# Kernel optimization log

Measured on AMD Instinct MI355X. Metric: run time of the kernel, lower is better.

The kernel has to match this reference:

```python
import jax, jax.numpy as jnp
import numpy as np

B, V, W, H = 512, 256, 64, 64  # batch, num_variables, window, hidden_size


def setup_inputs() -> dict:
    key = jax.random.key(0)
    ks = jax.random.split(key, 10)
    s = 0.05
    return {
        "x": jax.random.normal(ks[0], (B, V, W), dtype=jnp.float32),
        # nn.LSTM(input=V, hidden=H): gate order i, f, g, o
        "w_ih": jax.random.normal(ks[1], (4 * H, V), dtype=jnp.float32) * s,
        "w_hh": jax.random.normal(ks[2], (4 * H, H), dtype=jnp.float32) * s,
        "b_ih": jax.random.normal(ks[3], (4 * H,), dtype=jnp.float32) * s,
        "b_hh": jax.random.normal(ks[4], (4 * H,), dtype=jnp.float32) * s,
        # linear_v: Linear(window, 1, bias=False)
        "w_v": jax.random.normal(ks[5], (1, W), dtype=jnp.float32) * s,
        # linear_w: Linear(2H, window)
        "w_w": jax.random.normal(ks[6], (W, 2 * H), dtype=jnp.float32) * s,
        "b_w": jax.random.normal(ks[7], (W,), dtype=jnp.float32) * s,
        # linear_u: Linear(window, window)
        "w_u": jax.random.normal(ks[8], (W, W), dtype=jnp.float32) * s,
        "b_u": jax.random.normal(ks[9], (W,), dtype=jnp.float32) * s,
    }


def reference(x, w_ih, w_hh, b_ih, b_hh, w_v, w_w, b_w, w_u, b_u):
    batch, n_var, window = x.shape
    hidden = w_hh.shape[1]
    # linear_u over the window (last) dim: (B, V, W)
    u_out = jnp.einsum("bvw,uw->bvu", x, w_u) + b_u
    x_steps = jnp.transpose(x, (2, 0, 1))  # (W, B, V)

    def step(carry, x_t):
        h, c = carry  # each (B, H)
        # input attention
        wout = jnp.concatenate([h, c], axis=1) @ w_w.T + b_w          # (B, W)
        score = jnp.einsum("bvw,w->bv", jnp.tanh(wout[:, None, :] + u_out), w_v[0])
        alpha = jax.nn.softmax(score, axis=1)                          # (B, V)
        x_tilde = alpha * x_t                                          # (B, V)
        # LSTM cell (torch gate order i, f, g, o)
        gates = x_tilde @ w_ih.T + b_ih + h @ w_hh.T + b_hh            # (B, 4H)
        i_g, f_g, g_g, o_g = jnp.split(gates, 4, axis=1)
        i_g = jax.nn.sigmoid(i_g)
        f_g = jax.nn.sigmoid(f_g)
        g_g = jnp.tanh(g_g)
        o_g = jax.nn.sigmoid(o_g)
        c_new = f_g * c + i_g * g_g
        h_new = o_g * jnp.tanh(c_new)
        return (h_new, c_new), (x_tilde, h_new)

    init = (jnp.zeros((batch, hidden), x.dtype), jnp.zeros((batch, hidden), x.dtype))
    _, (x_tilde_seq, h_seq) = jax.lax.scan(step, init, x_steps)
    # matches torch.stack(x_tilde_list) (W,B,V) and torch.stack(h_list) (W,B,H)
    return x_tilde_seq, h_seq
```

## Files before the change

### kernel.cpp

```cpp
#include <hip/hip_runtime.h>


#define KLOG2E  1.4426950408889634f
#define K2LOG2E 2.8853900817779268f

typedef _Float16 h2 __attribute__((ext_vector_type(2)));
union H2U { h2 h; unsigned u; };

__device__ __forceinline__ float frcp(float x)  { return __builtin_amdgcn_rcpf(x); }
__device__ __forceinline__ float fexp2(float x) { return __builtin_amdgcn_exp2f(x); }
__device__ __forceinline__ float fsigmoid(float x) { return frcp(1.f + fexp2(-KLOG2E * x)); }
__device__ __forceinline__ float ftanh(float x) { return 1.f - 2.f * frcp(fexp2(K2LOG2E * x) + 1.f); }

#if __has_builtin(__builtin_amdgcn_fdot2)
__device__ __forceinline__ float fdot2(h2 a, h2 b, float c) { return __builtin_amdgcn_fdot2(a, b, c, false); }
#else
__device__ __forceinline__ float fdot2(h2 a, h2 b, float c) { return c + (float)a.x*(float)b.x + (float)a.y*(float)b.y; }
#endif

__device__ __forceinline__ h2 pkrtz(float a, float b) {
#if __has_builtin(__builtin_amdgcn_cvt_pkrtz)
    return __builtin_bit_cast(h2, __builtin_amdgcn_cvt_pkrtz(a, b));
#else
    h2 r; r.x = (_Float16)a; r.y = (_Float16)b; return r;
#endif
}

#define L_EA   0
#define L_EB   17408
#define L_PSA  34816
#define L_PSB  36864
#define L_XTA  38912
#define L_XTB  39168
#define L_XHA  39424
#define L_XHB  39552
#define L_EWA  39680
#define L_EWB  39744
#define L_HCA  39808
#define L_HCB  39936
#define L_BI   40064
#define L_WV   40320
#define L_TOT  40384

__global__ __launch_bounds__(512, 2) void enc_kernel(
    const float* __restrict__ x,
    const float* __restrict__ w_ih,
    const float* __restrict__ w_hh,
    const float* __restrict__ b_ih,
    const float* __restrict__ b_hh,
    const float* __restrict__ w_v,
    const float* __restrict__ w_w,
    const float* __restrict__ b_w,
    const float* __restrict__ w_u,
    const float* __restrict__ b_u,
    float* __restrict__ out_xt,
    float* __restrict__ out_h)
{
    extern __shared__ float lds[];
    float* EA  = lds + L_EA;   float* EB  = lds + L_EB;
    float* psA = lds + L_PSA;  float* psB = lds + L_PSB;
    float* xtA = lds + L_XTA;  float* xtB = lds + L_XTB;
    float* xhA = lds + L_XHA;  float* xhB = lds + L_XHB;
    float* ewA = lds + L_EWA;  float* ewB = lds + L_EWB;
    float* hcA = lds + L_HCA;  float* hcB = lds + L_HCB;
    float* biasL = lds + L_BI;
    float* wv2L  = lds + L_WV;

    const int tid  = threadIdx.x;
    const int lane = tid & 63;
    const int wvi  = tid >> 6;
    const int bA   = blockIdx.x;
    const int bB   = blockIdx.x + 256;

    h2    wihr2[64];
    float whhr[32];
    {
        const int jg = lane, sg = wvi;
#pragma unroll
        for (int jj = 0; jj < 4; ++jj) {
            const float4* g4 = (const float4*)(w_ih + (jg + 64*jj)*256 + sg*32);
#pragma unroll
            for (int i = 0; i < 8; ++i) {
                float4 v4 = g4[i];
                wihr2[jj*16 + 2*i + 0] = pkrtz(v4.x, v4.y);
                wihr2[jj*16 + 2*i + 1] = pkrtz(v4.z, v4.w);
            }
            const float4* h4 = (const float4*)(w_hh + (jg + 64*jj)*64 + sg*8);
            float4 u0 = h4[0], u1 = h4[1];
            whhr[jj*8 + 0] = u0.x; whhr[jj*8 + 1] = u0.y;
            whhr[jj*8 + 2] = u0.z; whhr[jj*8 + 3] = u0.w;
            whhr[jj*8 + 4] = u1.x; whhr[jj*8 + 5] = u1.y;
            whhr[jj*8 + 6] = u1.z; whhr[jj*8 + 7] = u1.w;
        }
    }
    const int w8 = wvi*8 + (lane & 7);
    const int kg = lane >> 3;
    float4 www4[4];
#pragma unroll
    for (int m = 0; m < 4; ++m)
        www4[m] = *(const float4*)&w_w[w8*128 + kg*4 + 32*m];
    const float bwr = b_w[w8];
    float Sv = 0.f;
#pragma unroll
    for (int wi = 0; wi < 64; ++wi) Sv += w_v[wi];
    const float bu_lane = b_u[lane];

    if (tid < 256) biasL[tid] = b_ih[tid] + b_hh[tid];
    if (tid < 64) wv2L[tid] = -2.f * w_v[tid];
    if (tid < 128) hcA[tid] = 0.f;
    else if (tid < 256) hcB[tid - 128] = 0.f;

#pragma unroll 1
    for (int bb = 0; bb < 2; ++bb) {
        float* E = bb ? EB : EA;
        const int b = bb ? bB : bA;
#pragma unroll 1
        for (int half = 0; half < 2; ++half) {
            float4 wu_r[8];
#pragma unroll
            for (int i = 0; i < 8; ++i)
                wu_r[i] = *(const float4*)&w_u[lane*64 + half*32 + 4*i];
            const float* xb = x + b*16384 + half*32;
#pragma unroll 2
            for (int vi = 0; vi < 32; ++vi) {
                int v = __builtin_amdgcn_readfirstlane(wvi*32 + vi);
                const float4* xr = (const float4*)(xb + v*64);
                float acc = 0.f;
#pragma unroll
                for (int i = 0; i < 8; ++i) {
                    float4 xx = xr[i]; float4 wu = wu_r[i];
                    acc += xx.x*wu.x + xx.y*wu.y + xx.z*wu.z + xx.w*wu.w;
                }
                if (half == 0) E[v*68 + lane] = acc + bu_lane;
                else           E[v*68 + lane] = fexp2(K2LOG2E * (E[v*68 + lane] + acc));
            }
        }
    }
    __syncthreads();

    const int  xj   = tid & 255;
    const int  bsel = tid >> 8;
    const float* xrow = x + (bsel ? bB : bA)*16384 + xj*64;
    float*       psX  = bsel ? psB : psA;
    const float* Erow = (bsel ? EB : EA) + xj*68;
    const float* ewX  = bsel ? ewB : ewA;
    float xcur = xrow[0];

    for (int t = 0; t < 64; ++t) {
        {
            float accA = 0.f, accB = 0.f;
#pragma unroll
            for (int m = 0; m < 4; ++m) {
                float4 w4 = www4[m];
                float4 hA = *(const float4*)&hcA[kg*4 + 32*m];
                float4 hB = *(const float4*)&hcB[kg*4 + 32*m];
                accA += hA.x*w4.x + hA.y*w4.y + hA.z*w4.z + hA.w*w4.w;
                accB += hB.x*w4.x + hB.y*w4.y + hB.z*w4.z + hB.w*w4.w;
            }
#pragma unroll
            for (int off = 8; off <= 32; off <<= 1) {
                accA += __shfl_xor(accA, off, 64);
                accB += __shfl_xor(accB, off, 64);
            }
            if (kg == 0)      ewA[w8] = fexp2(K2LOG2E * (accA + bwr));
            else if (kg == 1) ewB[w8] = fexp2(K2LOG2E * (accB + bwr));
        }
        float xnxt = (t < 63) ? xrow[t + 1] : 0.f;
        __syncthreads();

        {
            float acc = Sv;
#pragma unroll
            for (int q = 0; q < 16; ++q) {
                float4 e4 = *(const float4*)&Erow[4*q];
                float4 c4 = *(const float4*)&ewX[4*q];
                float4 v4 = *(const float4*)&wv2L[4*q];
                acc += v4.x * frcp(e4.x*c4.x + 1.f);
                acc += v4.y * frcp(e4.y*c4.y + 1.f);
                acc += v4.z * frcp(e4.z*c4.z + 1.f);
                acc += v4.w * frcp(e4.w*c4.w + 1.f);
            }
            float e = fexp2(KLOG2E * acc);
            psX[xj]       = e;
            psX[256 + xj] = e * xcur;
        }
        xcur = xnxt;
        __syncthreads();

        if (wvi < 2) {
            float* ps = wvi ? psB : psA;
            float* xt = wvi ? xtB : xtA;
            unsigned* xh = (unsigned*)(wvi ? xhB : xhA);
            float4 ev = *(const float4*)&ps[4*lane];
            float4 ex = *(const float4*)&ps[256 + 4*lane];
            float sum = (ev.x + ev.y) + (ev.z + ev.w);
#pragma unroll
            for (int off = 1; off <= 32; off <<= 1) sum += __shfl_xor(sum, off, 64);
            float r = frcp(sum);
            float4 xo;
            xo.x = ex.x*r; xo.y = ex.y*r; xo.z = ex.z*r; xo.w = ex.w*r;
            *(float4*)&xt[4*lane] = xo;
            H2U p0, p1;
            p0.h = pkrtz(xo.x, xo.y);
            p1.h = pkrtz(xo.z, xo.w);
            xh[2*lane]     = p0.u;
            xh[2*lane + 1] = p1.u;
        }
        __syncthreads();

        {
            float xtv = bsel ? xtB[xj] : xtA[xj];
            out_xt[t*131072 + (bsel ? bB : bA)*256 + xj] = xtv;

            const int sg = wvi, jg = lane;
            float aA[4] = {0.f, 0.f, 0.f, 0.f};
            float aB[4] = {0.f, 0.f, 0.f, 0.f};
            const uint4* xA = (const uint4*)xhA + sg*4;
            const uint4* xB = (const uint4*)xhB + sg*4;
#pragma unroll
            for (int i = 0; i < 4; ++i) {
                uint4 ua = xA[i], ub = xB[i];
                H2U u0, u1, u2, u3, v0, v1, v2, v3;
                u0.u = ua.x; u1.u = ua.y; u2.u = ua.z; u3.u = ua.w;
                v0.u = ub.x; v1.u = ub.y; v2.u = ub.z; v3.u = ub.w;
#pragma unroll
                for (int jj = 0; jj < 4; ++jj) {
                    aA[jj] = fdot2(u0.h, wihr2[jj*16 + 4*i + 0], aA[jj]);
                    aA[jj] = fdot2(u1.h, wihr2[jj*16 + 4*i + 1], aA[jj]);
                    aA[jj] = fdot2(u2.h, wihr2[jj*16 + 4*i + 2], aA[jj]);
                    aA[jj] = fdot2(u3.h, wihr2[jj*16 + 4*i + 3], aA[jj]);
                    aB[jj] = fdot2(v0.h, wihr2[jj*16 + 4*i + 0], aB[jj]);
                    aB[jj] = fdot2(v1.h, wihr2[jj*16 + 4*i + 1], aB[jj]);
                    aB[jj] = fdot2(v2.h, wihr2[jj*16 + 4*i + 2], aB[jj]);
                    aB[jj] = fdot2(v3.h, wihr2[jj*16 + 4*i + 3], aB[jj]);
                }
            }
            float4 hA0 = *(const float4*)&hcA[sg*8];
            float4 hA1 = *(const float4*)&hcA[sg*8 + 4];
            float4 hB0 = *(const float4*)&hcB[sg*8];
            float4 hB1 = *(const float4*)&hcB[sg*8 + 4];
#pragma unroll
            for (int jj = 0; jj < 4; ++jj) {
                aA[jj] += hA0.x*whhr[jj*8+0] + hA0.y*whhr[jj*8+1] + hA0.z*whhr[jj*8+2] + hA0.w*whhr[jj*8+3]
                        + hA1.x*whhr[jj*8+4] + hA1.y*whhr[jj*8+5] + hA1.z*whhr[jj*8+6] + hA1.w*whhr[jj*8+7];
                aB[jj] += hB0.x*whhr[jj*8+0] + hB0.y*whhr[jj*8+1] + hB0.z*whhr[jj*8+2] + hB0.w*whhr[jj*8+3]
                        + hB1.x*whhr[jj*8+4] + hB1.y*whhr[jj*8+5] + hB1.z*whhr[jj*8+6] + hB1.w*whhr[jj*8+7];
            }
            psA[sg*256 + jg      ] = aA[0];
            psA[sg*256 + jg +  64] = aA[1];
            psA[sg*256 + jg + 128] = aA[2];
            psA[sg*256 + jg + 192] = aA[3];
            psB[sg*256 + jg      ] = aB[0];
            psB[sg*256 + jg +  64] = aB[1];
            psB[sg*256 + jg + 128] = aB[2];
            psB[sg*256 + jg + 192] = aB[3];
        }
        __syncthreads();

        if (wvi < 2) {
            float* ps = wvi ? psB : psA;
            float* hc = wvi ? hcB : hcA;
            float* oh = out_h + t*32768 + (wvi ? bB : bA)*64;
            const int k = lane;
            float gi = biasL[k], gf = biasL[64+k], gg = biasL[128+k], go = biasL[192+k];
#pragma unroll
            for (int s = 0; s < 8; ++s) {
                gi += ps[s*256 + k      ];
                gf += ps[s*256 + k +  64];
                gg += ps[s*256 + k + 128];
                go += ps[s*256 + k + 192];
            }
            gi = fsigmoid(gi); gf = fsigmoid(gf);
            gg = ftanh(gg);    go = fsigmoid(go);
            float cn = gf * hc[64 + k] + gi * gg;
            float hn = go * ftanh(cn);
            hc[k] = hn; hc[64 + k] = cn;
            oh[k] = hn;
        }
        __syncthreads();
    }
}

extern "C" void kernel_launch(void* const* d_in, const int* in_sizes, int n_in,
                              void* d_out, int out_size, void* d_ws, size_t ws_size,
                              hipStream_t stream) {
    const float* x    = (const float*)d_in[0];
    const float* w_ih = (const float*)d_in[1];
    const float* w_hh = (const float*)d_in[2];
    const float* b_ih = (const float*)d_in[3];
    const float* b_hh = (const float*)d_in[4];
    const float* w_v  = (const float*)d_in[5];
    const float* w_w  = (const float*)d_in[6];
    const float* b_w  = (const float*)d_in[7];
    const float* w_u  = (const float*)d_in[8];
    const float* b_u  = (const float*)d_in[9];

    float* out_xt = (float*)d_out;
    float* out_h  = out_xt + 64*512*256;

    const size_t shbytes = (size_t)L_TOT * sizeof(float);
    (void)hipFuncSetAttribute((const void*)enc_kernel,
                        hipFuncAttributeMaxDynamicSharedMemorySize, (int)shbytes);
    enc_kernel<<<dim3(256), dim3(512), shbytes, stream>>>(
        x, w_ih, w_hh, b_ih, b_hh, w_v, w_w, b_w, w_u, b_u, out_xt, out_h);
}
```

Measured before the change: 305.9 us.

## Assign one batch per block, fuse softmax normalization into gate matvec, fp16 w_hh

Each block now handles a single batch element instead of two, and the grid grows to 512 blocks with a higher occupancy hint and much smaller LDS use. The softmax sum is reduced inside the score phase and the normalization is applied after the w_ih dot product, which removes one barrier-separated phase per step. The split-K over the gate matvec changes from 8 wave groups to 2 thread halves, so each thread computes a full gate column over 128 inputs. w_hh and h now go through fp16 packed dot products, and w_ih is converted with round-to-nearest instead of round-toward-zero. The x_tilde fed to the LSTM is now unnormalized fp16 before scaling, which changes rounding and adds a risk of fp16 overflow.

```diff
diff --git a/kernel.cpp b/kernel.cpp
--- a/kernel.cpp
+++ b/kernel.cpp
@@ -18,31 +18,30 @@
 __device__ __forceinline__ float fdot2(h2 a, h2 b, float c) { return c + (float)a.x*(float)b.x + (float)a.y*(float)b.y; }
 #endif
 
-__device__ __forceinline__ h2 pkrtz(float a, float b) {
+__device__ __forceinline__ unsigned pkrtz_u(float a, float b) {
 #if __has_builtin(__builtin_amdgcn_cvt_pkrtz)
-    return __builtin_bit_cast(h2, __builtin_amdgcn_cvt_pkrtz(a, b));
+    H2U r; r.h = __builtin_bit_cast(h2, __builtin_amdgcn_cvt_pkrtz(a, b)); return r.u;
 #else
+    H2U r; r.h.x = (_Float16)a; r.h.y = (_Float16)b; return r.u;
+#endif
+}
+__device__ __forceinline__ h2 pk_rtn(float a, float b) {
     h2 r; r.x = (_Float16)a; r.y = (_Float16)b; return r;
-#endif
-}
-
-#define L_EA   0
-#define L_EB   17408
-#define L_PSA  34816
-#define L_PSB  36864
-#define L_XTA  38912
-#define L_XTB  39168
-#define L_XHA  39424
-#define L_XHB  39552
-#define L_EWA  39680
-#define L_EWB  39744
-#define L_HCA  39808
-#define L_HCB  39936
-#define L_BI   40064
-#define L_WV   40320
-#define L_TOT  40384
-
-__global__ __launch_bounds__(512, 2) void enc_kernel(
+}
+
+#define L_E    0
+#define L_PS   17408
+#define L_EXF  17920
+#define L_XH   18176
+#define L_EW   18304
+#define L_HC   18368
+#define L_HCH  18496
+#define L_BI   18528
+#define L_WV   18784
+#define L_WS   18848
+#define L_TOT  18856
+
+__global__ __launch_bounds__(512, 4) void enc_kernel(
     const float* __restrict__ x,
     const float* __restrict__ w_ih,
     const float* __restrict__ w_hh,
@@ -57,40 +56,75 @@
     float* __restrict__ out_h)
 {
     extern __shared__ float lds[];
-    float* EA  = lds + L_EA;   float* EB  = lds + L_EB;
-    float* psA = lds + L_PSA;  float* psB = lds + L_PSB;
-    float* xtA = lds + L_XTA;  float* xtB = lds + L_XTB;
-    float* xhA = lds + L_XHA;  float* xhB = lds + L_XHB;
-    float* ewA = lds + L_EWA;  float* ewB = lds + L_EWB;
-    float* hcA = lds + L_HCA;  float* hcB = lds + L_HCB;
-    float* biasL = lds + L_BI;
-    float* wv2L  = lds + L_WV;
+    float*    E     = lds + L_E;
+    float*    ps    = lds + L_PS;
+    float*    exf   = lds + L_EXF;
+    unsigned* xh    = (unsigned*)(lds + L_XH);
+    float*    ew    = lds + L_EW;
+    float*    hc    = lds + L_HC;
+    unsigned* hch   = (unsigned*)(lds + L_HCH);
+    float*    biasL = lds + L_BI;
+    float*    wv2L  = lds + L_WV;
+    float*    wsum  = lds + L_WS;
 
     const int tid  = threadIdx.x;
     const int lane = tid & 63;
     const int wvi  = tid >> 6;
-    const int bA   = blockIdx.x;
-    const int bB   = blockIdx.x + 256;
-
-    h2    wihr2[64];
-    float whhr[32];
+    const int b    = blockIdx.x;
+    const int j    = tid & 255;
+    const int sg   = tid >> 8;
+
+    if (tid < 256) biasL[tid] = b_ih[tid] + b_hh[tid];
+    if (tid < 64)  wv2L[tid] = -2.f * w_v[tid];
+    if (tid < 128) hc[tid] = 0.f;
+    if (tid < 32)  hch[tid] = 0u;
+
+    float Sv = 0.f;
+#pragma unroll
+    for (int wi = 0; wi < 64; ++wi) Sv += w_v[wi];
+    const float bu_lane = b_u[lane];
+
+#pragma unroll 1
+    for (int half = 0; half < 2; ++half) {
+        float4 wu_r[8];
+#pragma unroll
+        for (int i = 0; i < 8; ++i)
+            wu_r[i] = *(const float4*)&w_u[lane*64 + half*32 + 4*i];
+        const float* xb = x + b*16384 + half*32;
+#pragma unroll 2
+        for (int vi = 0; vi < 32; ++vi) {
+            int v = __builtin_amdgcn_readfirstlane(wvi*32 + vi);
+            const float4* xr = (const float4*)(xb + v*64);
+            float acc = 0.f;
+#pragma unroll
+            for (int i = 0; i < 8; ++i) {
+                float4 xx = xr[i]; float4 wu = wu_r[i];
+                acc += xx.x*wu.x + xx.y*wu.y + xx.z*wu.z + xx.w*wu.w;
+            }
+            if (half == 0) E[v*68 + lane] = acc + bu_lane;
+            else           E[v*68 + lane] = fexp2(K2LOG2E * (E[v*68 + lane] + acc));
+        }
+    }
+    __syncthreads();
+
+    h2 wihr2[64];
     {
-        const int jg = lane, sg = wvi;
-#pragma unroll
-        for (int jj = 0; jj < 4; ++jj) {
-            const float4* g4 = (const float4*)(w_ih + (jg + 64*jj)*256 + sg*32);
-#pragma unroll
-            for (int i = 0; i < 8; ++i) {
-                float4 v4 = g4[i];
-                wihr2[jj*16 + 2*i + 0] = pkrtz(v4.x, v4.y);
-                wihr2[jj*16 + 2*i + 1] = pkrtz(v4.z, v4.w);
-            }
-            const float4* h4 = (const float4*)(w_hh + (jg + 64*jj)*64 + sg*8);
-            float4 u0 = h4[0], u1 = h4[1];
-            whhr[jj*8 + 0] = u0.x; whhr[jj*8 + 1] = u0.y;
-            whhr[jj*8 + 2] = u0.z; whhr[jj*8 + 3] = u0.w;
-            whhr[jj*8 + 4] = u1.x; whhr[jj*8 + 5] = u1.y;
-            whhr[jj*8 + 6] = u1.z; whhr[jj*8 + 7] = u1.w;
+        const float4* g4 = (const float4*)(w_ih + j*256 + sg*128);
+#pragma unroll
+        for (int i = 0; i < 32; ++i) {
+            float4 v4 = g4[i];
+            wihr2[2*i]     = pk_rtn(v4.x, v4.y);
+            wihr2[2*i + 1] = pk_rtn(v4.z, v4.w);
+        }
+    }
+    h2 whh2[16];
+    {
+        const float4* h4 = (const float4*)(w_hh + j*64 + sg*32);
+#pragma unroll
+        for (int i = 0; i < 8; ++i) {
+            float4 v4 = h4[i];
+            whh2[2*i]     = pk_rtn(v4.x, v4.y);
+            whh2[2*i + 1] = pk_rtn(v4.z, v4.w);
         }
     }
     const int w8 = wvi*8 + (lane & 7);
@@ -100,182 +134,99 @@
     for (int m = 0; m < 4; ++m)
         www4[m] = *(const float4*)&w_w[w8*128 + kg*4 + 32*m];
     const float bwr = b_w[w8];
-    float Sv = 0.f;
-#pragma unroll
-    for (int wi = 0; wi < 64; ++wi) Sv += w_v[wi];
-    const float bu_lane = b_u[lane];
-
-    if (tid < 256) biasL[tid] = b_ih[tid] + b_hh[tid];
-    if (tid < 64) wv2L[tid] = -2.f * w_v[tid];
-    if (tid < 128) hcA[tid] = 0.f;
-    else if (tid < 256) hcB[tid - 128] = 0.f;
-
-#pragma unroll 1
-    for (int bb = 0; bb < 2; ++bb) {
-        float* E = bb ? EB : EA;
-        const int b = bb ? bB : bA;
-#pragma unroll 1
-        for (int half = 0; half < 2; ++half) {
-            float4 wu_r[8];
-#pragma unroll
-            for (int i = 0; i < 8; ++i)
-                wu_r[i] = *(const float4*)&w_u[lane*64 + half*32 + 4*i];
-            const float* xb = x + b*16384 + half*32;
-#pragma unroll 2
-            for (int vi = 0; vi < 32; ++vi) {
-                int v = __builtin_amdgcn_readfirstlane(wvi*32 + vi);
-                const float4* xr = (const float4*)(xb + v*64);
-                float acc = 0.f;
-#pragma unroll
-                for (int i = 0; i < 8; ++i) {
-                    float4 xx = xr[i]; float4 wu = wu_r[i];
-                    acc += xx.x*wu.x + xx.y*wu.y + xx.z*wu.z + xx.w*wu.w;
-                }
-                if (half == 0) E[v*68 + lane] = acc + bu_lane;
-                else           E[v*68 + lane] = fexp2(K2LOG2E * (E[v*68 + lane] + acc));
-            }
-        }
-    }
-    __syncthreads();
-
-    const int  xj   = tid & 255;
-    const int  bsel = tid >> 8;
-    const float* xrow = x + (bsel ? bB : bA)*16384 + xj*64;
-    float*       psX  = bsel ? psB : psA;
-    const float* Erow = (bsel ? EB : EA) + xj*68;
-    const float* ewX  = bsel ? ewB : ewA;
+
+    const float* xrow = x + b*16384 + j*64;
     float xcur = xrow[0];
 
     for (int t = 0; t < 64; ++t) {
         {
-            float accA = 0.f, accB = 0.f;
+            float acc = 0.f;
 #pragma unroll
             for (int m = 0; m < 4; ++m) {
                 float4 w4 = www4[m];
-                float4 hA = *(const float4*)&hcA[kg*4 + 32*m];
-                float4 hB = *(const float4*)&hcB[kg*4 + 32*m];
-                accA += hA.x*w4.x + hA.y*w4.y + hA.z*w4.z + hA.w*w4.w;
-                accB += hB.x*w4.x + hB.y*w4.y + hB.z*w4.z + hB.w*w4.w;
-            }
-#pragma unroll
-            for (int off = 8; off <= 32; off <<= 1) {
-                accA += __shfl_xor(accA, off, 64);
-                accB += __shfl_xor(accB, off, 64);
-            }
-            if (kg == 0)      ewA[w8] = fexp2(K2LOG2E * (accA + bwr));
-            else if (kg == 1) ewB[w8] = fexp2(K2LOG2E * (accB + bwr));
+                float4 hv = *(const float4*)&hc[kg*4 + 32*m];
+                acc += hv.x*w4.x + hv.y*w4.y + hv.z*w4.z + hv.w*w4.w;
+            }
+#pragma unroll
+            for (int off = 8; off <= 32; off <<= 1)
+                acc += __shfl_xor(acc, off, 64);
+            if (kg == 0) ew[w8] = fexp2(K2LOG2E * (acc + bwr));
         }
         float xnxt = (t < 63) ? xrow[t + 1] : 0.f;
         __syncthreads();
 
-        {
+        if (tid < 256) {
             float acc = Sv;
+            const float* Erow = E + j*68;
 #pragma unroll
             for (int q = 0; q < 16; ++q) {
                 float4 e4 = *(const float4*)&Erow[4*q];
-                float4 c4 = *(const float4*)&ewX[4*q];
+                float4 c4 = *(const float4*)&ew[4*q];
                 float4 v4 = *(const float4*)&wv2L[4*q];
                 acc += v4.x * frcp(e4.x*c4.x + 1.f);
                 acc += v4.y * frcp(e4.y*c4.y + 1.f);
                 acc += v4.z * frcp(e4.z*c4.z + 1.f);
                 acc += v4.w * frcp(e4.w*c4.w + 1.f);
             }
-            float e = fexp2(KLOG2E * acc);
-            psX[xj]       = e;
-            psX[256 + xj] = e * xcur;
+            float e  = fexp2(KLOG2E * acc);
+            float ex = e * xcur;
+            float s = e;
+#pragma unroll
+            for (int off = 1; off <= 32; off <<= 1) s += __shfl_xor(s, off, 64);
+            if (lane == 0) wsum[wvi] = s;
+            exf[j] = ex;
+            float exp2v = __shfl_xor(ex, 1, 64);
+            if (!(lane & 1)) xh[j >> 1] = pkrtz_u(ex, exp2v);
         }
         xcur = xnxt;
         __syncthreads();
 
-        if (wvi < 2) {
-            float* ps = wvi ? psB : psA;
-            float* xt = wvi ? xtB : xtA;
-            unsigned* xh = (unsigned*)(wvi ? xhB : xhA);
-            float4 ev = *(const float4*)&ps[4*lane];
-            float4 ex = *(const float4*)&ps[256 + 4*lane];
-            float sum = (ev.x + ev.y) + (ev.z + ev.w);
-#pragma unroll
-            for (int off = 1; off <= 32; off <<= 1) sum += __shfl_xor(sum, off, 64);
-            float r = frcp(sum);
-            float4 xo;
-            xo.x = ex.x*r; xo.y = ex.y*r; xo.z = ex.z*r; xo.w = ex.w*r;
-            *(float4*)&xt[4*lane] = xo;
-            H2U p0, p1;
-            p0.h = pkrtz(xo.x, xo.y);
-            p1.h = pkrtz(xo.z, xo.w);
-            xh[2*lane]     = p0.u;
-            xh[2*lane + 1] = p1.u;
-        }
-        __syncthreads();
-
         {
-            float xtv = bsel ? xtB[xj] : xtA[xj];
-            out_xt[t*131072 + (bsel ? bB : bA)*256 + xj] = xtv;
-
-            const int sg = wvi, jg = lane;
-            float aA[4] = {0.f, 0.f, 0.f, 0.f};
-            float aB[4] = {0.f, 0.f, 0.f, 0.f};
-            const uint4* xA = (const uint4*)xhA + sg*4;
-            const uint4* xB = (const uint4*)xhB + sg*4;
+            float r = frcp(wsum[0] + wsum[1] + wsum[2] + wsum[3]);
+            if (sg == 0) out_xt[t*131072 + b*256 + j] = r * exf[j];
+
+            float a = 0.f;
+            const uint4* xx = (const uint4*)xh + sg*16;
+#pragma unroll
+            for (int i = 0; i < 16; ++i) {
+                uint4 u = xx[i];
+                H2U p0, p1, p2, p3;
+                p0.u = u.x; p1.u = u.y; p2.u = u.z; p3.u = u.w;
+                a = fdot2(p0.h, wihr2[4*i + 0], a);
+                a = fdot2(p1.h, wihr2[4*i + 1], a);
+                a = fdot2(p2.h, wihr2[4*i + 2], a);
+                a = fdot2(p3.h, wihr2[4*i + 3], a);
+            }
+            float ah = 0.f;
+            const uint4* hh = (const uint4*)hch + sg*4;
 #pragma unroll
             for (int i = 0; i < 4; ++i) {
-                uint4 ua = xA[i], ub = xB[i];
-                H2U u0, u1, u2, u3, v0, v1, v2, v3;
-                u0.u = ua.x; u1.u = ua.y; u2.u = ua.z; u3.u = ua.w;
-                v0.u = ub.x; v1.u = ub.y; v2.u = ub.z; v3.u = ub.w;
-#pragma unroll
-                for (int jj = 0; jj < 4; ++jj) {
-                    aA[jj] = fdot2(u0.h, wihr2[jj*16 + 4*i + 0], aA[jj]);
-                    aA[jj] = fdot2(u1.h, wihr2[jj*16 + 4*i + 1], aA[jj]);
-                    aA[jj] = fdot2(u2.h, wihr2[jj*16 + 4*i + 2], aA[jj]);
-                    aA[jj] = fdot2(u3.h, wihr2[jj*16 + 4*i + 3], aA[jj]);
-                    aB[jj] = fdot2(v0.h, wihr2[jj*16 + 4*i + 0], aB[jj]);
-                    aB[jj] = fdot2(v1.h, wihr2[jj*16 + 4*i + 1], aB[jj]);
-                    aB[jj] = fdot2(v2.h, wihr2[jj*16 + 4*i + 2], aB[jj]);
-                    aB[jj] = fdot2(v3.h, wihr2[jj*16 + 4*i + 3], aB[jj]);
-                }
-            }
-            float4 hA0 = *(const float4*)&hcA[sg*8];
-            float4 hA1 = *(const float4*)&hcA[sg*8 + 4];
-            float4 hB0 = *(const float4*)&hcB[sg*8];
-            float4 hB1 = *(const float4*)&hcB[sg*8 + 4];
-#pragma unroll
-            for (int jj = 0; jj < 4; ++jj) {
-                aA[jj] += hA0.x*whhr[jj*8+0] + hA0.y*whhr[jj*8+1] + hA0.z*whhr[jj*8+2] + hA0.w*whhr[jj*8+3]
-                        + hA1.x*whhr[jj*8+4] + hA1.y*whhr[jj*8+5] + hA1.z*whhr[jj*8+6] + hA1.w*whhr[jj*8+7];
-                aB[jj] += hB0.x*whhr[jj*8+0] + hB0.y*whhr[jj*8+1] + hB0.z*whhr[jj*8+2] + hB0.w*whhr[jj*8+3]
-                        + hB1.x*whhr[jj*8+4] + hB1.y*whhr[jj*8+5] + hB1.z*whhr[jj*8+6] + hB1.w*whhr[jj*8+7];
-            }
-            psA[sg*256 + jg      ] = aA[0];
-            psA[sg*256 + jg +  64] = aA[1];
-            psA[sg*256 + jg + 128] = aA[2];
-            psA[sg*256 + jg + 192] = aA[3];
-            psB[sg*256 + jg      ] = aB[0];
-            psB[sg*256 + jg +  64] = aB[1];
-            psB[sg*256 + jg + 128] = aB[2];
-            psB[sg*256 + jg + 192] = aB[3];
-        }
-        __syncthreads();
-
-        if (wvi < 2) {
-            float* ps = wvi ? psB : psA;
-            float* hc = wvi ? hcB : hcA;
-            float* oh = out_h + t*32768 + (wvi ? bB : bA)*64;
+                uint4 u = hh[i];
+                H2U p0, p1, p2, p3;
+                p0.u = u.x; p1.u = u.y; p2.u = u.z; p3.u = u.w;
+                ah = fdot2(p0.h, whh2[4*i + 0], ah);
+                ah = fdot2(p1.h, whh2[4*i + 1], ah);
+                ah = fdot2(p2.h, whh2[4*i + 2], ah);
+                ah = fdot2(p3.h, whh2[4*i + 3], ah);
+            }
+            ps[sg*256 + j] = r*a + ah;
+        }
+        __syncthreads();
+
+        if (wvi == 0) {
             const int k = lane;
-            float gi = biasL[k], gf = biasL[64+k], gg = biasL[128+k], go = biasL[192+k];
-#pragma unroll
-            for (int s = 0; s < 8; ++s) {
-                gi += ps[s*256 + k      ];
-                gf += ps[s*256 + k +  64];
-                gg += ps[s*256 + k + 128];
-                go += ps[s*256 + k + 192];
-            }
+            float gi = biasL[k      ] + ps[k      ] + ps[256 + k      ];
+            float gf = biasL[64  + k] + ps[64  + k] + ps[256 + 64  + k];
+            float gg = biasL[128 + k] + ps[128 + k] + ps[256 + 128 + k];
+            float go = biasL[192 + k] + ps[192 + k] + ps[256 + 192 + k];
             gi = fsigmoid(gi); gf = fsigmoid(gf);
             gg = ftanh(gg);    go = fsigmoid(go);
             float cn = gf * hc[64 + k] + gi * gg;
             float hn = go * ftanh(cn);
             hc[k] = hn; hc[64 + k] = cn;
-            oh[k] = hn;
+            float hp = __shfl_xor(hn, 1, 64);
+            if (!(lane & 1)) hch[k >> 1] = pkrtz_u(hn, hp);
+            out_h[t*32768 + b*64 + k] = hn;
         }
         __syncthreads();
     }
@@ -301,6 +252,6 @@
     const size_t shbytes = (size_t)L_TOT * sizeof(float);
     (void)hipFuncSetAttribute((const void*)enc_kernel,
                         hipFuncAttributeMaxDynamicSharedMemorySize, (int)shbytes);
-    enc_kernel<<<dim3(256), dim3(512), shbytes, stream>>>(
+    enc_kernel<<<dim3(512), dim3(512), shbytes, stream>>>(
         x, w_ih, w_hh, b_ih, b_hh, w_v, w_w, b_w, w_u, b_u, out_xt, out_h);
 }
```

New measurement: 845.4 us. 176% more time.

## Fold softmax normalization into gate matmul and remove a barrier stage

Applied to the files above, without the earlier changes.

The separate softmax-normalization stage, run by two waves between barriers, is removed. Each wave now reduces its partial exp sums into a small LDS array and packs unnormalized e*x values to fp16 directly. The reciprocal of the sum is applied after the w_ih dot product and when writing out_xt. This cuts one __syncthreads and a serial two-wave phase from each of the 64 timesteps. It also splits accumulators to shorten dependency chains, converts w_ih with round-to-nearest, and changes fp16 rounding because the values are packed before normalization, which alters precision.

```diff
diff --git a/kernel.cpp b/kernel.cpp
--- a/kernel.cpp
+++ b/kernel.cpp
@@ -18,20 +18,23 @@
 __device__ __forceinline__ float fdot2(h2 a, h2 b, float c) { return c + (float)a.x*(float)b.x + (float)a.y*(float)b.y; }
 #endif
 
-__device__ __forceinline__ h2 pkrtz(float a, float b) {
+__device__ __forceinline__ unsigned pkrtz_u(float a, float b) {
 #if __has_builtin(__builtin_amdgcn_cvt_pkrtz)
-    return __builtin_bit_cast(h2, __builtin_amdgcn_cvt_pkrtz(a, b));
+    H2U r; r.h = __builtin_bit_cast(h2, __builtin_amdgcn_cvt_pkrtz(a, b)); return r.u;
 #else
+    H2U r; r.h.x = (_Float16)a; r.h.y = (_Float16)b; return r.u;
+#endif
+}
+__device__ __forceinline__ h2 pk_rtn(float a, float b) {
     h2 r; r.x = (_Float16)a; r.y = (_Float16)b; return r;
-#endif
 }
 
 #define L_EA   0
 #define L_EB   17408
 #define L_PSA  34816
 #define L_PSB  36864
-#define L_XTA  38912
-#define L_XTB  39168
+#define L_EXFA 38912
+#define L_EXFB 39168
 #define L_XHA  39424
 #define L_XHB  39552
 #define L_EWA  39680
@@ -40,7 +43,8 @@
 #define L_HCB  39936
 #define L_BI   40064
 #define L_WV   40320
-#define L_TOT  40384
+#define L_WS   40384
+#define L_TOT  40392
 
 __global__ __launch_bounds__(512, 2) void enc_kernel(
     const float* __restrict__ x,
@@ -57,14 +61,16 @@
     float* __restrict__ out_h)
 {
     extern __shared__ float lds[];
-    float* EA  = lds + L_EA;   float* EB  = lds + L_EB;
-    float* psA = lds + L_PSA;  float* psB = lds + L_PSB;
-    float* xtA = lds + L_XTA;  float* xtB = lds + L_XTB;
-    float* xhA = lds + L_XHA;  float* xhB = lds + L_XHB;
-    float* ewA = lds + L_EWA;  float* ewB = lds + L_EWB;
-    float* hcA = lds + L_HCA;  float* hcB = lds + L_HCB;
-    float* biasL = lds + L_BI;
-    float* wv2L  = lds + L_WV;
+    float*    EA   = lds + L_EA;    float*    EB   = lds + L_EB;
+    float*    psA  = lds + L_PSA;   float*    psB  = lds + L_PSB;
+    float*    exfA = lds + L_EXFA;  float*    exfB = lds + L_EXFB;
+    unsigned* xhA  = (unsigned*)(lds + L_XHA);
+    unsigned* xhB  = (unsigned*)(lds + L_XHB);
+    float*    ewA  = lds + L_EWA;   float*    ewB  = lds + L_EWB;
+    float*    hcA  = lds + L_HCA;   float*    hcB  = lds + L_HCB;
+    float*    biasL= lds + L_BI;
+    float*    wv2L = lds + L_WV;
+    float*    wsum = lds + L_WS;
 
     const int tid  = threadIdx.x;
     const int lane = tid & 63;
@@ -82,8 +88,8 @@
 #pragma unroll
             for (int i = 0; i < 8; ++i) {
                 float4 v4 = g4[i];
-                wihr2[jj*16 + 2*i + 0] = pkrtz(v4.x, v4.y);
-                wihr2[jj*16 + 2*i + 1] = pkrtz(v4.z, v4.w);
+                wihr2[jj*16 + 2*i + 0] = pk_rtn(v4.x, v4.y);
+                wihr2[jj*16 + 2*i + 1] = pk_rtn(v4.z, v4.w);
             }
             const float4* h4 = (const float4*)(w_hh + (jg + 64*jj)*64 + sg*8);
             float4 u0 = h4[0], u1 = h4[1];
@@ -107,8 +113,7 @@
 
     if (tid < 256) biasL[tid] = b_ih[tid] + b_hh[tid];
     if (tid < 64) wv2L[tid] = -2.f * w_v[tid];
-    if (tid < 128) hcA[tid] = 0.f;
-    else if (tid < 256) hcB[tid - 128] = 0.f;
+    if (tid < 128) { hcA[tid] = 0.f; hcB[tid] = 0.f; }
 
 #pragma unroll 1
     for (int bb = 0; bb < 2; ++bb) {
@@ -141,9 +146,10 @@
     const int  xj   = tid & 255;
     const int  bsel = tid >> 8;
     const float* xrow = x + (bsel ? bB : bA)*16384 + xj*64;
-    float*       psX  = bsel ? psB : psA;
     const float* Erow = (bsel ? EB : EA) + xj*68;
     const float* ewX  = bsel ? ewB : ewA;
+    float*       exfX = bsel ? exfB : exfA;
+    unsigned*    xhX  = bsel ? xhB : xhA;
     float xcur = xrow[0];
 
     for (int t = 0; t < 64; ++t) {
@@ -169,57 +175,44 @@
         __syncthreads();
 
         {
-            float acc = Sv;
+            float ac0 = 0.f, ac1 = 0.f, ac2 = 0.f, ac3 = 0.f;
 #pragma unroll
             for (int q = 0; q < 16; ++q) {
                 float4 e4 = *(const float4*)&Erow[4*q];
                 float4 c4 = *(const float4*)&ewX[4*q];
                 float4 v4 = *(const float4*)&wv2L[4*q];
-                acc += v4.x * frcp(e4.x*c4.x + 1.f);
-                acc += v4.y * frcp(e4.y*c4.y + 1.f);
-                acc += v4.z * frcp(e4.z*c4.z + 1.f);
-                acc += v4.w * frcp(e4.w*c4.w + 1.f);
-            }
-            float e = fexp2(KLOG2E * acc);
-            psX[xj]       = e;
-            psX[256 + xj] = e * xcur;
+                ac0 += v4.x * frcp(e4.x*c4.x + 1.f);
+                ac1 += v4.y * frcp(e4.y*c4.y + 1.f);
+                ac2 += v4.z * frcp(e4.z*c4.z + 1.f);
+                ac3 += v4.w * frcp(e4.w*c4.w + 1.f);
+            }
+            float acc = Sv + ((ac0 + ac1) + (ac2 + ac3));
+            float e  = fexp2(KLOG2E * acc);
+            float ex = e * xcur;
+            float s = e;
+#pragma unroll
+            for (int off = 1; off <= 32; off <<= 1) s += __shfl_xor(s, off, 64);
+            if (lane == 0) wsum[wvi] = s;
+            exfX[xj] = ex;
+            float ex2 = __shfl_xor(ex, 1, 64);
+            if (!(lane & 1)) xhX[xj >> 1] = pkrtz_u(ex, ex2);
         }
         xcur = xnxt;
         __syncthreads();
 
-        if (wvi < 2) {
-            float* ps = wvi ? psB : psA;
-            float* xt = wvi ? xtB : xtA;
-            unsigned* xh = (unsigned*)(wvi ? xhB : xhA);
-            float4 ev = *(const float4*)&ps[4*lane];
-            float4 ex = *(const float4*)&ps[256 + 4*lane];
-            float sum = (ev.x + ev.y) + (ev.z + ev.w);
-#pragma unroll
-            for (int off = 1; off <= 32; off <<= 1) sum += __shfl_xor(sum, off, 64);
-            float r = frcp(sum);
-            float4 xo;
-            xo.x = ex.x*r; xo.y = ex.y*r; xo.z = ex.z*r; xo.w = ex.w*r;
-            *(float4*)&xt[4*lane] = xo;
-            H2U p0, p1;
-            p0.h = pkrtz(xo.x, xo.y);
-            p1.h = pkrtz(xo.z, xo.w);
-            xh[2*lane]     = p0.u;
-            xh[2*lane + 1] = p1.u;
-        }
-        __syncthreads();
-
         {
-            float xtv = bsel ? xtB[xj] : xtA[xj];
-            out_xt[t*131072 + (bsel ? bB : bA)*256 + xj] = xtv;
+            float rA = frcp((wsum[0] + wsum[1]) + (wsum[2] + wsum[3]));
+            float rB = frcp((wsum[4] + wsum[5]) + (wsum[6] + wsum[7]));
+            out_xt[t*131072 + (bsel ? bB : bA)*256 + xj] = (bsel ? rB : rA) * exfX[xj];
 
             const int sg = wvi, jg = lane;
             float aA[4] = {0.f, 0.f, 0.f, 0.f};
             float aB[4] = {0.f, 0.f, 0.f, 0.f};
-            const uint4* xA = (const uint4*)xhA + sg*4;
-            const uint4* xB = (const uint4*)xhB + sg*4;
+            const uint4* xxA = (const uint4*)xhA + sg*4;
+            const uint4* xxB = (const uint4*)xhB + sg*4;
 #pragma unroll
             for (int i = 0; i < 4; ++i) {
-                uint4 ua = xA[i], ub = xB[i];
+                uint4 ua = xxA[i], ub = xxB[i];
                 H2U u0, u1, u2, u3, v0, v1, v2, v3;
                 u0.u = ua.x; u1.u = ua.y; u2.u = ua.z; u3.u = ua.w;
                 v0.u = ub.x; v1.u = ub.y; v2.u = ub.z; v3.u = ub.w;
@@ -241,19 +234,17 @@
             float4 hB1 = *(const float4*)&hcB[sg*8 + 4];
 #pragma unroll
             for (int jj = 0; jj < 4; ++jj) {
-                aA[jj] += hA0.x*whhr[jj*8+0] + hA0.y*whhr[jj*8+1] + hA0.z*whhr[jj*8+2] + hA0.w*whhr[jj*8+3]
-                        + hA1.x*whhr[jj*8+4] + hA1.y*whhr[jj*8+5] + hA1.z*whhr[jj*8+6] + hA1.w*whhr[jj*8+7];
-                aB[jj] += hB0.x*whhr[jj*8+0] + hB0.y*whhr[jj*8+1] + hB0.z*whhr[jj*8+2] + hB0.w*whhr[jj*8+3]
-                        + hB1.x*whhr[jj*8+4] + hB1.y*whhr[jj*8+5] + hB1.z*whhr[jj*8+6] + hB1.w*whhr[jj*8+7];
-            }
-            psA[sg*256 + jg      ] = aA[0];
-            psA[sg*256 + jg +  64] = aA[1];
-            psA[sg*256 + jg + 128] = aA[2];
-            psA[sg*256 + jg + 192] = aA[3];
-            psB[sg*256 + jg      ] = aB[0];
-            psB[sg*256 + jg +  64] = aB[1];
-            psB[sg*256 + jg + 128] = aB[2];
-            psB[sg*256 + jg + 192] = aB[3];
+                float hhA = (hA0.x*whhr[jj*8+0] + hA0.y*whhr[jj*8+1])
+                          + (hA0.z*whhr[jj*8+2] + hA0.w*whhr[jj*8+3])
+                          + (hA1.x*whhr[jj*8+4] + hA1.y*whhr[jj*8+5])
+                          + (hA1.z*whhr[jj*8+6] + hA1.w*whhr[jj*8+7]);
+                float hhB = (hB0.x*whhr[jj*8+0] + hB0.y*whhr[jj*8+1])
+                          + (hB0.z*whhr[jj*8+2] + hB0.w*whhr[jj*8+3])
+                          + (hB1.x*whhr[jj*8+4] + hB1.y*whhr[jj*8+5])
+                          + (hB1.z*whhr[jj*8+6] + hB1.w*whhr[jj*8+7]);
+                psA[sg*256 + jg + 64*jj] = rA*aA[jj] + hhA;
+                psB[sg*256 + jg + 64*jj] = rB*aB[jj] + hhB;
+            }
         }
         __syncthreads();
 
@@ -262,14 +253,18 @@
             float* hc = wvi ? hcB : hcA;
             float* oh = out_h + t*32768 + (wvi ? bB : bA)*64;
             const int k = lane;
-            float gi = biasL[k], gf = biasL[64+k], gg = biasL[128+k], go = biasL[192+k];
-#pragma unroll
-            for (int s = 0; s < 8; ++s) {
-                gi += ps[s*256 + k      ];
-                gf += ps[s*256 + k +  64];
-                gg += ps[s*256 + k + 128];
-                go += ps[s*256 + k + 192];
-            }
+            float gi = biasL[k] +
+                (((ps[0*256 + k] + ps[1*256 + k]) + (ps[2*256 + k] + ps[3*256 + k])) +
+                 ((ps[4*256 + k] + ps[5*256 + k]) + (ps[6*256 + k] + ps[7*256 + k])));
+            float gf = biasL[64 + k] +
+                (((ps[0*256 + 64 + k] + ps[1*256 + 64 + k]) + (ps[2*256 + 64 + k] + ps[3*256 + 64 + k])) +
+                 ((ps[4*256 + 64 + k] + ps[5*256 + 64 + k]) + (ps[6*256 + 64 + k] + ps[7*256 + 64 + k])));
+            float gg = biasL[128 + k] +
+                (((ps[0*256 + 128 + k] + ps[1*256 + 128 + k]) + (ps[2*256 + 128 + k] + ps[3*256 + 128 + k])) +
+                 ((ps[4*256 + 128 + k] + ps[5*256 + 128 + k]) + (ps[6*256 + 128 + k] + ps[7*256 + 128 + k])));
+            float go = biasL[192 + k] +
+                (((ps[0*256 + 192 + k] + ps[1*256 + 192 + k]) + (ps[2*256 + 192 + k] + ps[3*256 + 192 + k])) +
+                 ((ps[4*256 + 192 + k] + ps[5*256 + 192 + k]) + (ps[6*256 + 192 + k] + ps[7*256 + 192 + k])));
             gi = fsigmoid(gi); gf = fsigmoid(gf);
             gg = ftanh(gg);    go = fsigmoid(go);
             float cn = gf * hc[64 + k] + gi * gg;
```

After: 314.1 us. +2.7%, slower.
